# Optimization experiments

Hardware: AMD Instinct MI355X
Metric: run time of the kernel (lower is better)

The kernel has to match this reference:

```python
import jax, jax.numpy as jnp
import numpy as np

NKV = 8      # n_head_kv
G = 8        # n_head // n_head_kv
D = 64       # head_dim (hardcoded in source views)
NH = NKV * G # n_head = 64


def rotate_half(x):
    x1, x2 = x[..., : D // 2], x[..., D // 2:]
    return jnp.concatenate((-x2, x1), axis=-1)


def setup_inputs() -> dict:
    key = jax.random.key(0)
    ks = jax.random.split(key, 9)
    B, S, H = 2, 1024, 4096
    hidden_states = jax.random.normal(ks[0], (B, S, H), dtype=jnp.float32)
    alibi = jnp.zeros((B * NH, 1, S), dtype=jnp.float32)            # unused in this forward path
    attention_mask = jnp.zeros((B, 1, S, S), dtype=jnp.float32)      # unused (is_causal=True)
    cos = jax.random.uniform(ks[1], (S, D), dtype=jnp.float32, minval=-1.0, maxval=1.0)
    sin = jax.random.uniform(ks[2], (S, D), dtype=jnp.float32, minval=-1.0, maxval=1.0)
    wq = jax.random.normal(ks[3], (H, H), dtype=jnp.float32) * 0.02          # Linear weight (out, in)
    wk = jax.random.normal(ks[4], (NKV * D, H), dtype=jnp.float32) * 0.02
    wv = jax.random.normal(ks[5], (NKV * D, H), dtype=jnp.float32) * 0.02
    wd = jax.random.normal(ks[6], (H, H), dtype=jnp.float32) * 0.02          # dense weight
    return {"hidden_states": hidden_states, "alibi": alibi, "attention_mask": attention_mask,
            "cos": cos, "sin": sin, "wq": wq, "wk": wk, "wv": wv, "wd": wd}


def reference(hidden_states, alibi, attention_mask, cos, sin, wq, wk, wv, wd):
    B, S, H = hidden_states.shape
    # fused-style projections (Linear: x @ W.T, no bias)
    # q: [B, S, NKV, G, D] -> [B, NKV, G, S, D]; head h = kv_group*G + j (group-major, matches source rearrange)
    q = (hidden_states @ wq.T).reshape(B, S, NKV, G, D).transpose(0, 2, 3, 1, 4)
    k = (hidden_states @ wk.T).reshape(B, S, NKV, D).transpose(0, 2, 1, 3)   # [B, NKV, S, D]
    v = (hidden_states @ wv.T).reshape(B, S, NKV, D).transpose(0, 2, 1, 3)
    # RoPE (cos/sin broadcast over batch/head dims)
    q = q * cos + rotate_half(q) * sin
    k = k * cos + rotate_half(k) * sin
    # grouped-query attention without materializing broadcast K/V
    inv_norm = jnp.asarray(1.0 / np.sqrt(D), dtype=hidden_states.dtype)
    scores = jnp.einsum('bkgsd,bktd->bkgst', q, k) * inv_norm        # [B, NKV, G, S, S]
    causal = jnp.tril(jnp.ones((S, S), dtype=bool))
    neg = jnp.finfo(scores.dtype).min
    scores = jnp.where(causal, scores, scores + neg)
    probs = jax.nn.softmax(scores, axis=-1)
    out = jnp.einsum('bkgst,bktd->bkgsd', probs, v)                  # [B, NKV, G, S, D]
    out = out.reshape(B, NH, S, D).transpose(0, 2, 1, 3).reshape(B, S, NH * D)
    return out @ wd.T
```

## Files before the change

### kernel.cpp

```cpp
#include <hip/hip_runtime.h>
#include <hip/hip_bf16.h>
#include <cstdint>

typedef short short8 __attribute__((ext_vector_type(8)));
typedef __bf16 bf16x8 __attribute__((ext_vector_type(8)));
typedef float float4v __attribute__((ext_vector_type(4)));
typedef float float16v __attribute__((ext_vector_type(16)));

#define NKV 8
#define G 8
#define D 64
#define NH 64
#define BB 2
#define S 1024
#define H 4096
#define MROWS (BB*S)
#define NQKV (H + 2*NKV*D)

__device__ __forceinline__ unsigned short f2b(float f) {
    union { float f; uint32_t u; } v; v.f = f;
    uint32_t u = v.u;
    uint32_t r = (u + 0x7FFFu + ((u >> 16) & 1u)) >> 16;
    return (unsigned short)r;
}
__device__ __forceinline__ float b2f(unsigned short b) {
    union { float f; uint32_t u; } v; v.u = ((uint32_t)b) << 16;
    return v.f;
}

__device__ __forceinline__ void gload_lds16(const unsigned short* g, unsigned short* l) {
    __builtin_amdgcn_global_load_lds(
        (const __attribute__((address_space(1))) uint32_t*)g,
        (__attribute__((address_space(3))) uint32_t*)l, 16, 0, 0);
}

__global__ void cvt_all(const float* __restrict__ hs, const float* __restrict__ wq,
                        const float* __restrict__ wk, const float* __restrict__ wv,
                        const float* __restrict__ wd,
                        unsigned short* __restrict__ hs_b, unsigned short* __restrict__ wqkv_b,
                        unsigned short* __restrict__ wd_b) {
    const size_t N0 = (size_t)MROWS * H;
    const size_t N1 = (size_t)H * H;
    const size_t N2 = (size_t)512 * H;
    const size_t N3 = (size_t)512 * H;
    const size_t N4 = (size_t)H * H;
    const size_t total4 = (N0 + N1 + N2 + N3 + N4) / 4;
    size_t i = (size_t)blockIdx.x * blockDim.x + threadIdx.x;
    const size_t stride = (size_t)gridDim.x * blockDim.x;
    for (; i < total4; i += stride) {
        size_t e = i * 4;
        const float* s; unsigned short* d;
        if (e < N0)                { s = hs + e;                  d = hs_b + e; }
        else if (e < N0+N1)        { s = wq + (e-N0);             d = wqkv_b + (e-N0); }
        else if (e < N0+N1+N2)     { s = wk + (e-N0-N1);          d = wqkv_b + N1 + (e-N0-N1); }
        else if (e < N0+N1+N2+N3)  { s = wv + (e-N0-N1-N2);       d = wqkv_b + N1+N2 + (e-N0-N1-N2); }
        else                       { s = wd + (e-N0-N1-N2-N3);    d = wd_b + (e-N0-N1-N2-N3); }
        float4 f = *(const float4*)s;
        ushort4 o;
        o.x = f2b(f.x); o.y = f2b(f.y); o.z = f2b(f.z); o.w = f2b(f.w);
        *(ushort4*)d = o;
    }
}

template <bool BF16_OUT>
__global__ __launch_bounds__(256) void gemm_nt(
    const unsigned short* __restrict__ A, const unsigned short* __restrict__ W,
    void* __restrict__ Cv, int M, int N, int K) {
    __shared__ unsigned short As[128 * 32];
    __shared__ unsigned short Bs[128 * 32];
    const int bm = blockIdx.y * 128, bn = blockIdx.x * 128;
    const int tid = threadIdx.x;
    const int w = tid >> 6, lane = tid & 63;
    const int n32 = lane & 31, khalf = lane >> 5;
    const int wm = (w & 1) * 64, wn = (w >> 1) * 64;

    const int r0 = tid >> 2;
    const int c0 = (tid & 3) ^ ((r0 >> 2) & 3);
    const unsigned short* pA0 = A + (size_t)(bm + r0) * K + c0 * 8;
    const unsigned short* pA1 = A + (size_t)(bm + r0 + 64) * K + c0 * 8;
    const unsigned short* pW0 = W + (size_t)(bn + r0) * K + c0 * 8;
    const unsigned short* pW1 = W + (size_t)(bn + r0 + 64) * K + c0 * 8;
    unsigned short* Asl0 = As + tid * 8;
    unsigned short* Asl1 = As + 2048 + tid * 8;
    unsigned short* Bsl0 = Bs + tid * 8;
    unsigned short* Bsl1 = Bs + 2048 + tid * 8;

    const unsigned short* aP[2][2];
    const unsigned short* bP[2][2];
#pragma unroll
    for (int g = 0; g < 2; g++)
#pragma unroll
        for (int s = 0; s < 2; s++) {
            int cp = ((s << 1) | khalf) ^ ((n32 >> 2) & 3);
            aP[g][s] = &As[(wm + g * 32 + n32) * 32 + cp * 8];
            bP[g][s] = &Bs[(wn + g * 32 + n32) * 32 + cp * 8];
        }

    float16v acc[2][2] = {};

    const int iters = K >> 5;
    for (int it = 0; it < iters; ++it) {
        __syncthreads();
        gload_lds16(pA0, Asl0);
        gload_lds16(pA1, Asl1);
        gload_lds16(pW0, Bsl0);
        gload_lds16(pW1, Bsl1);
        pA0 += 32; pA1 += 32; pW0 += 32; pW1 += 32;
        __syncthreads();
        bf16x8 af[2][2], bf[2][2];
#pragma unroll
        for (int g = 0; g < 2; g++)
#pragma unroll
            for (int s = 0; s < 2; s++) {
                af[g][s] = *(const bf16x8*)aP[g][s];
                bf[g][s] = *(const bf16x8*)bP[g][s];
            }
#pragma unroll
        for (int s = 0; s < 2; s++)
#pragma unroll
            for (int mg = 0; mg < 2; mg++)
#pragma unroll
                for (int ng = 0; ng < 2; ng++)
                    acc[mg][ng] = __builtin_amdgcn_mfma_f32_32x32x16_bf16(
                        af[mg][s], bf[ng][s], acc[mg][ng], 0, 0, 0);
    }

#pragma unroll
    for (int mg = 0; mg < 2; mg++) {
#pragma unroll
        for (int ng = 0; ng < 2; ng++) {
            int gcol = bn + wn + ng * 32 + n32;
#pragma unroll
            for (int reg = 0; reg < 16; reg++) {
                int grow = bm + wm + mg * 32 + (reg & 3) + 8 * (reg >> 2) + 4 * khalf;
                if (BF16_OUT)
                    ((unsigned short*)Cv)[(size_t)grow * N + gcol] = f2b(acc[mg][ng][reg]);
                else
                    ((float*)Cv)[(size_t)grow * N + gcol] = acc[mg][ng][reg];
            }
        }
    }
}

__global__ void rope_scatter(const unsigned short* __restrict__ qkv,
                             const float* __restrict__ cosb, const float* __restrict__ sinb,
                             unsigned short* __restrict__ qa, unsigned short* __restrict__ ka,
                             unsigned short* __restrict__ vt) {
    int idx = blockIdx.x * blockDim.x + threadIdx.x;
    const int total = MROWS * NQKV;
    const int stride = gridDim.x * blockDim.x;
    for (; idx < total; idx += stride) {
        int row = idx / NQKV, o = idx - row * NQKV;
        int b = row >> 10, s = row & 1023;
        float x = b2f(qkv[idx]);
        if (o < H) {
            int kv = o >> 9, g = (o >> 6) & 7, d = o & 63;
            int po = (d < 32) ? idx + 32 : idx - 32;
            float partner = b2f(qkv[po]);
            float rot = (d < 32) ? -partner : partner;
            float y = x * cosb[s * 64 + d] + rot * sinb[s * 64 + d];
            int h = b * 64 + kv * 8 + g;
            qa[(size_t)h * (S * D) + s * 64 + d] = f2b(y);
        } else if (o < H + 512) {
            int o2 = o - H;
            int kv = o2 >> 6, d = o2 & 63;
            int po = (d < 32) ? idx + 32 : idx - 32;
            float partner = b2f(qkv[po]);
            float rot = (d < 32) ? -partner : partner;
            float y = x * cosb[s * 64 + d] + rot * sinb[s * 64 + d];
            ka[(size_t)(b * NKV + kv) * (S * D) + s * 64 + d] = f2b(y);
        } else {
            int o2 = o - H - 512;
            int kv = o2 >> 6, d = o2 & 63;
            vt[(size_t)(b * NKV + kv) * (D * S) + (size_t)d * S + s] = qkv[idx];
        }
    }
}

__global__ __launch_bounds__(256) void attn_kernel(
    const unsigned short* __restrict__ qa, const unsigned short* __restrict__ ka,
    const unsigned short* __restrict__ vt, unsigned short* __restrict__ out) {
    __shared__ unsigned short Ps[4 * 16 * 72];
    const int p = blockIdx.x;
    const int yy = blockIdx.y;
    const int b = yy >> 5, kvh = (yy >> 2) & 7, gp = yy & 3;
    const int h0 = b * 64 + kvh * 8 + gp * 2;
    const int tid = threadIdx.x, w = tid >> 6, lane = tid & 63;
    const int col = lane & 15, quad = lane >> 4;
    const unsigned short* Kg = ka + (size_t)(b * NKV + kvh) * (S * D);
    const unsigned short* Vg = vt + (size_t)(b * NKV + kvh) * (D * S);
    float4v zero4 = {0.f, 0.f, 0.f, 0.f};
    const float SC2 = 0.125f * 1.44269504089f;

#pragma unroll
    for (int part = 0; part < 2; part++) {
        const int qt = part ? (15 - p) : p;
        const int qb = qt * 64;

        bf16x8 aq[2][2];
#pragma unroll
        for (int hd = 0; hd < 2; hd++)
#pragma unroll
            for (int c = 0; c < 2; c++)
                aq[hd][c] = *(const bf16x8*)&qa[(size_t)(h0 + hd) * (S * D) + (size_t)qb * D
                                               + (w * 16 + col) * 64 + c * 32 + quad * 8];

        float m_run[2][4], l_run[2][4];
        float4v o_acc[2][4];
#pragma unroll
        for (int hd = 0; hd < 2; hd++) {
#pragma unroll
            for (int r = 0; r < 4; r++) { m_run[hd][r] = -1e30f; l_run[hd][r] = 0.f; }
#pragma unroll
            for (int dg = 0; dg < 4; dg++) o_acc[hd][dg] = zero4;
        }

        for (int kt = 0; kt <= qt; kt++) {
            const int kb = kt * 64;
            bf16x8 bk[4][2], bv[4][2];
#pragma unroll
            for (int n16 = 0; n16 < 4; n16++) {
                const unsigned short* kr = &Kg[(size_t)(kb + n16 * 16 + col) * 64 + quad * 8];
                bk[n16][0] = *(const bf16x8*)kr;
                bk[n16][1] = *(const bf16x8*)(kr + 32);
            }
#pragma unroll
            for (int dg = 0; dg < 4; dg++) {
                const unsigned short* vr = &Vg[(size_t)(dg * 16 + col) * S + kb + quad * 8];
                bv[dg][0] = *(const bf16x8*)vr;
                bv[dg][1] = *(const bf16x8*)(vr + 32);
            }

#pragma unroll
            for (int hd = 0; hd < 2; hd++) {
                float4v sc[4];
                __builtin_amdgcn_s_setprio(1);
#pragma unroll
                for (int n16 = 0; n16 < 4; n16++) {
                    float4v a = __builtin_amdgcn_mfma_f32_16x16x32_bf16(aq[hd][0], bk[n16][0], zero4, 0, 0, 0);
                    sc[n16] = __builtin_amdgcn_mfma_f32_16x16x32_bf16(aq[hd][1], bk[n16][1], a, 0, 0, 0);
                }
                __builtin_amdgcn_s_setprio(0);
#pragma unroll
                for (int n16 = 0; n16 < 4; n16++) {
                    int key = kb + n16 * 16 + col;
#pragma unroll
                    for (int r = 0; r < 4; r++) {
                        int qrow = qb + w * 16 + quad * 4 + r;
                        float sv = sc[n16][r] * SC2;
                        sc[n16][r] = (key <= qrow) ? sv : -1e30f;
                    }
                }
#pragma unroll
                for (int r = 0; r < 4; r++) {
                    float mx = fmaxf(fmaxf(sc[0][r], sc[1][r]), fmaxf(sc[2][r], sc[3][r]));
#pragma unroll
                    for (int off = 1; off < 16; off <<= 1) mx = fmaxf(mx, __shfl_xor(mx, off));
                    float mnew = fmaxf(m_run[hd][r], mx);
                    float alpha = __builtin_amdgcn_exp2f(m_run[hd][r] - mnew);
                    float rsum = 0.f;
#pragma unroll
                    for (int n16 = 0; n16 < 4; n16++) {
                        float pr = __builtin_amdgcn_exp2f(sc[n16][r] - mnew);
                        sc[n16][r] = pr;
                        rsum += pr;
                    }
#pragma unroll
                    for (int off = 1; off < 16; off <<= 1) rsum += __shfl_xor(rsum, off);
                    l_run[hd][r] = l_run[hd][r] * alpha + rsum;
                    m_run[hd][r] = mnew;
#pragma unroll
                    for (int dg = 0; dg < 4; dg++) o_acc[hd][dg][r] *= alpha;
                }
#pragma unroll
                for (int n16 = 0; n16 < 4; n16++)
#pragma unroll
                    for (int r = 0; r < 4; r++)
                        Ps[w * 1152 + (quad * 4 + r) * 72 + n16 * 16 + col] = f2b(sc[n16][r]);
                bf16x8 ap[2];
#pragma unroll
                for (int c = 0; c < 2; c++)
                    ap[c] = *(const bf16x8*)&Ps[w * 1152 + col * 72 + c * 32 + quad * 8];
                __builtin_amdgcn_s_setprio(1);
#pragma unroll
                for (int dg = 0; dg < 4; dg++) {
                    float4v t = __builtin_amdgcn_mfma_f32_16x16x32_bf16(ap[0], bv[dg][0], o_acc[hd][dg], 0, 0, 0);
                    o_acc[hd][dg] = __builtin_amdgcn_mfma_f32_16x16x32_bf16(ap[1], bv[dg][1], t, 0, 0, 0);
                }
                __builtin_amdgcn_s_setprio(0);
            }
        }
#pragma unroll
        for (int hd = 0; hd < 2; hd++) {
            const int hcol = ((h0 + hd) & 63) * 64;
#pragma unroll
            for (int r = 0; r < 4; r++) {
                float inv = 1.f / l_run[hd][r];
                int grow = b * S + qb + w * 16 + quad * 4 + r;
#pragma unroll
                for (int dg = 0; dg < 4; dg++)
                    out[(size_t)grow * H + hcol + dg * 16 + col] = f2b(o_acc[hd][dg][r] * inv);
            }
        }
    }
}

extern "C" void kernel_launch(void* const* d_in, const int* in_sizes, int n_in,
                              void* d_out, int out_size, void* d_ws, size_t ws_size,
                              hipStream_t stream) {
    const float* hs   = (const float*)d_in[0];
    const float* cosb = (const float*)d_in[3];
    const float* sinb = (const float*)d_in[4];
    const float* wq   = (const float*)d_in[5];
    const float* wk   = (const float*)d_in[6];
    const float* wv   = (const float*)d_in[7];
    const float* wd   = (const float*)d_in[8];

    char* p = (char*)d_ws;
    auto alloc = [&](size_t bytes) { char* r = p; p += (bytes + 255) & ~(size_t)255; return r; };
    unsigned short* wqkv_b = (unsigned short*)alloc((size_t)NQKV * H * 2);
    unsigned short* wd_b   = (unsigned short*)alloc((size_t)H * H * 2);
    unsigned short* qkv    = (unsigned short*)alloc((size_t)MROWS * NQKV * 2);
    unsigned short* qa     = (unsigned short*)alloc((size_t)BB * NH * S * D * 2);
    unsigned short* ka     = (unsigned short*)alloc((size_t)BB * NKV * S * D * 2);
    unsigned short* vt     = (unsigned short*)alloc((size_t)BB * NKV * S * D * 2);
    unsigned short* hs_b   = (unsigned short*)alloc((size_t)MROWS * H * 2);
    unsigned short* ao     = hs_b;

    cvt_all<<<4096, 256, 0, stream>>>(hs, wq, wk, wv, wd, hs_b, wqkv_b, wd_b);

    gemm_nt<true><<<dim3(NQKV / 128, MROWS / 128), 256, 0, stream>>>(hs_b, wqkv_b, qkv, MROWS, NQKV, H);
    rope_scatter<<<4096, 256, 0, stream>>>(qkv, cosb, sinb, qa, ka, vt);
    attn_kernel<<<dim3(8, 64), 256, 0, stream>>>(qa, ka, vt, ao);
    gemm_nt<false><<<dim3(H / 128, MROWS / 128), 256, 0, stream>>>(ao, wd_b, d_out, MROWS, H, H);
}
```

Before: 486.3 us.

## Fuse RoPE and Q/K/V scatter into the QKV GEMM epilogue

Removes the separate rope_scatter kernel and the intermediate bf16 qkv buffer by applying RoPE in the QKV GEMM epilogue and writing q/k directly in head-major layout. For V tiles, the accumulator is staged transposed through enlarged shared memory and written to the transposed vt layout with vector stores. This saves a full write and read of the QKV intermediate plus one kernel launch. In exchange, the GEMM kernel uses more shared memory (about 34KB), which may reduce occupancy, and its epilogue stores are scattered.

```diff
diff --git a/kernel.cpp b/kernel.cpp
--- a/kernel.cpp
+++ b/kernel.cpp
@@ -62,12 +62,16 @@
     }
 }
 
-template <bool BF16_OUT>
+template <int MODE>
 __global__ __launch_bounds__(256) void gemm_nt(
     const unsigned short* __restrict__ A, const unsigned short* __restrict__ W,
-    void* __restrict__ Cv, int M, int N, int K) {
-    __shared__ unsigned short As[128 * 32];
-    __shared__ unsigned short Bs[128 * 32];
+    void* __restrict__ Cv, int M, int N, int K,
+    const float* __restrict__ cosb, const float* __restrict__ sinb,
+    unsigned short* __restrict__ qa, unsigned short* __restrict__ ka,
+    unsigned short* __restrict__ vt) {
+    __shared__ unsigned short sh[17408];
+    unsigned short* As = sh;
+    unsigned short* Bs = sh + 4096;
     const int bm = blockIdx.y * 128, bn = blockIdx.x * 128;
     const int tid = threadIdx.x;
     const int w = tid >> 6, lane = tid & 63;
@@ -125,54 +129,67 @@
                         af[mg][s], bf[ng][s], acc[mg][ng], 0, 0, 0);
     }
 
-#pragma unroll
-    for (int mg = 0; mg < 2; mg++) {
-#pragma unroll
-        for (int ng = 0; ng < 2; ng++) {
-            int gcol = bn + wn + ng * 32 + n32;
-#pragma unroll
-            for (int reg = 0; reg < 16; reg++) {
-                int grow = bm + wm + mg * 32 + (reg & 3) + 8 * (reg >> 2) + 4 * khalf;
-                if (BF16_OUT)
-                    ((unsigned short*)Cv)[(size_t)grow * N + gcol] = f2b(acc[mg][ng][reg]);
-                else
+    if (MODE == 0) {
+#pragma unroll
+        for (int mg = 0; mg < 2; mg++) {
+#pragma unroll
+            for (int ng = 0; ng < 2; ng++) {
+                int gcol = bn + wn + ng * 32 + n32;
+#pragma unroll
+                for (int reg = 0; reg < 16; reg++) {
+                    int grow = bm + wm + mg * 32 + (reg & 3) + 8 * (reg >> 2) + 4 * khalf;
                     ((float*)Cv)[(size_t)grow * N + gcol] = acc[mg][ng][reg];
-            }
-        }
-    }
-}
-
-__global__ void rope_scatter(const unsigned short* __restrict__ qkv,
-                             const float* __restrict__ cosb, const float* __restrict__ sinb,
-                             unsigned short* __restrict__ qa, unsigned short* __restrict__ ka,
-                             unsigned short* __restrict__ vt) {
-    int idx = blockIdx.x * blockDim.x + threadIdx.x;
-    const int total = MROWS * NQKV;
-    const int stride = gridDim.x * blockDim.x;
-    for (; idx < total; idx += stride) {
-        int row = idx / NQKV, o = idx - row * NQKV;
-        int b = row >> 10, s = row & 1023;
-        float x = b2f(qkv[idx]);
-        if (o < H) {
-            int kv = o >> 9, g = (o >> 6) & 7, d = o & 63;
-            int po = (d < 32) ? idx + 32 : idx - 32;
-            float partner = b2f(qkv[po]);
-            float rot = (d < 32) ? -partner : partner;
-            float y = x * cosb[s * 64 + d] + rot * sinb[s * 64 + d];
-            int h = b * 64 + kv * 8 + g;
-            qa[(size_t)h * (S * D) + s * 64 + d] = f2b(y);
-        } else if (o < H + 512) {
-            int o2 = o - H;
-            int kv = o2 >> 6, d = o2 & 63;
-            int po = (d < 32) ? idx + 32 : idx - 32;
-            float partner = b2f(qkv[po]);
-            float rot = (d < 32) ? -partner : partner;
-            float y = x * cosb[s * 64 + d] + rot * sinb[s * 64 + d];
-            ka[(size_t)(b * NKV + kv) * (S * D) + s * 64 + d] = f2b(y);
+                }
+            }
+        }
+    } else {
+        const int colbase = bn + wn;
+        if (bn < H + 512) {
+#pragma unroll
+            for (int mg = 0; mg < 2; mg++) {
+#pragma unroll
+                for (int reg = 0; reg < 16; reg++) {
+                    int grow = bm + wm + mg * 32 + (reg & 3) + 8 * (reg >> 2) + 4 * khalf;
+                    int s = grow & 1023, b = grow >> 10;
+                    float x0 = acc[mg][0][reg], x1 = acc[mg][1][reg];
+                    float c0  = cosb[s * 64 + n32],      sn0 = sinb[s * 64 + n32];
+                    float c1  = cosb[s * 64 + 32 + n32], sn1 = sinb[s * 64 + 32 + n32];
+                    unsigned short o0 = f2b(x0 * c0 - x1 * sn0);
+                    unsigned short o1 = f2b(x1 * c1 + x0 * sn1);
+                    unsigned short* dp;
+                    if (bn < H) {
+                        dp = qa + (size_t)(b * 64 + (colbase >> 6)) * (S * D) + s * 64 + n32;
+                    } else {
+                        dp = ka + (size_t)(b * 8 + ((colbase - H) >> 6)) * (S * D) + s * 64 + n32;
+                    }
+                    dp[0] = o0; dp[32] = o1;
+                }
+            }
         } else {
-            int o2 = o - H - 512;
-            int kv = o2 >> 6, d = o2 & 63;
-            vt[(size_t)(b * NKV + kv) * (D * S) + (size_t)d * S + s] = qkv[idx];
+            __syncthreads();
+#pragma unroll
+            for (int mg = 0; mg < 2; mg++)
+#pragma unroll
+                for (int ng = 0; ng < 2; ng++)
+#pragma unroll
+                    for (int reg = 0; reg < 16; reg++) {
+                        int cl = wn + ng * 32 + n32;
+                        int rl = wm + mg * 32 + (reg & 3) + 8 * (reg >> 2) + 4 * khalf;
+                        sh[cl * 136 + rl] = f2b(acc[mg][ng][reg]);
+                    }
+            __syncthreads();
+            {
+                const int bb = bm >> 10, s0 = bm & 1023;
+                const int kv0 = (bn - (H + 512)) >> 6;
+                const int cl = tid >> 1, shalf = (tid & 1) * 64;
+                const int kv = kv0 + (cl >> 6), dd = cl & 63;
+                unsigned short* dstp = vt + (size_t)(bb * 8 + kv) * (D * S)
+                                          + (size_t)dd * S + s0 + shalf;
+                const unsigned short* srcp = sh + cl * 136 + shalf;
+#pragma unroll
+                for (int j = 0; j < 8; j++)
+                    *(short8*)(dstp + j * 8) = *(const short8*)(srcp + j * 8);
+            }
         }
     }
 }
@@ -320,7 +337,6 @@
     auto alloc = [&](size_t bytes) { char* r = p; p += (bytes + 255) & ~(size_t)255; return r; };
     unsigned short* wqkv_b = (unsigned short*)alloc((size_t)NQKV * H * 2);
     unsigned short* wd_b   = (unsigned short*)alloc((size_t)H * H * 2);
-    unsigned short* qkv    = (unsigned short*)alloc((size_t)MROWS * NQKV * 2);
     unsigned short* qa     = (unsigned short*)alloc((size_t)BB * NH * S * D * 2);
     unsigned short* ka     = (unsigned short*)alloc((size_t)BB * NKV * S * D * 2);
     unsigned short* vt     = (unsigned short*)alloc((size_t)BB * NKV * S * D * 2);
@@ -329,8 +345,9 @@
 
     cvt_all<<<4096, 256, 0, stream>>>(hs, wq, wk, wv, wd, hs_b, wqkv_b, wd_b);
 
-    gemm_nt<true><<<dim3(NQKV / 128, MROWS / 128), 256, 0, stream>>>(hs_b, wqkv_b, qkv, MROWS, NQKV, H);
-    rope_scatter<<<4096, 256, 0, stream>>>(qkv, cosb, sinb, qa, ka, vt);
+    gemm_nt<1><<<dim3(NQKV / 128, MROWS / 128), 256, 0, stream>>>(
+        hs_b, wqkv_b, nullptr, MROWS, NQKV, H, cosb, sinb, qa, ka, vt);
     attn_kernel<<<dim3(8, 64), 256, 0, stream>>>(qa, ka, vt, ao);
-    gemm_nt<false><<<dim3(H / 128, MROWS / 128), 256, 0, stream>>>(ao, wd_b, d_out, MROWS, H, H);
-}
+    gemm_nt<0><<<dim3(H / 128, MROWS / 128), 256, 0, stream>>>(
+        ao, wd_b, d_out, MROWS, H, H, nullptr, nullptr, nullptr, nullptr, nullptr);
+}
```

Result: faster. 462.2 us (-4.9%).
